# Performance work log

Hardware: AMD Instinct MI355X
Metric: run time of the kernel (lower is better)

## Reference

```python
import jax, jax.numpy as jnp
import numpy as np

EMBED = 1024
HEADS = 16
HEAD_DIM = EMBED // HEADS
SCALE = HEAD_DIM ** -0.5


def setup_inputs() -> dict:
    key = jax.random.key(0)
    ks = jax.random.split(key, 9)
    init = lambda k, shape: jax.random.normal(k, shape, dtype=jnp.float32) * 0.02
    return {
        "hidden_states": jax.random.normal(ks[0], (32, 257, EMBED), dtype=jnp.float32),
        "Wq": init(ks[1], (EMBED, EMBED)), "bq": init(ks[2], (EMBED,)),
        "Wk": init(ks[3], (EMBED, EMBED)), "bk": init(ks[4], (EMBED,)),
        "Wv": init(ks[5], (EMBED, EMBED)), "bv": init(ks[6], (EMBED,)),
        "Wo": init(ks[7], (EMBED, EMBED)), "bo": init(ks[8], (EMBED,)),
    }


def reference(hidden_states, Wq, bq, Wk, bk, Wv, bv, Wo, bo):
    b, t, d = hidden_states.shape
    # projections (torch Linear: x @ W.T + b); scale applied to Q
    q = (hidden_states @ Wq.T + bq) * SCALE
    k = hidden_states @ Wk.T + bk
    v = hidden_states @ Wv.T + bv
    # [b, h, t, hd]
    q = q.reshape(b, t, HEADS, HEAD_DIM).transpose(0, 2, 1, 3)
    k = k.reshape(b, t, HEADS, HEAD_DIM).transpose(0, 2, 1, 3)
    v = v.reshape(b, t, HEADS, HEAD_DIM).transpose(0, 2, 1, 3)
    # attention scores + softmax (dropout p is a no-op in eval mode)
    scores = jnp.einsum("bhqd,bhkd->bhqk", q, k)
    probs = jax.nn.softmax(scores, axis=-1)
    ctx = jnp.einsum("bhqk,bhkd->bhqd", probs, v)
    ctx = ctx.transpose(0, 2, 1, 3).reshape(b, t, d)
    return ctx @ Wo.T + bo
```

## Files before the change

kernel.cpp:

```cpp
#include <hip/hip_runtime.h>


#define B_   32
#define T_   257
#define TP   272
#define H_   16
#define HD_  64
#define D_   1024
#define NTOK 8224
#define BH_  512
#define FRAG_PER_BH 17408

typedef __bf16 bf16;
typedef __bf16 bf16x4 __attribute__((ext_vector_type(4)));
typedef __bf16 bf16x8 __attribute__((ext_vector_type(8)));
typedef short  s16x4  __attribute__((ext_vector_type(4)));
typedef short  s16x8  __attribute__((ext_vector_type(8)));
typedef float  floatx4 __attribute__((ext_vector_type(4)));

static constexpr size_t SZ_XB   = (size_t)NTOK * D_ * 2;
static constexpr size_t SZ_WQKV = (size_t)3 * D_ * D_ * 2;
static constexpr size_t SZ_W    = (size_t)D_ * D_ * 2;
static constexpr size_t SZ_QK   = (size_t)BH_ * FRAG_PER_BH * 2;

static constexpr size_t OFF_XB   = 0;
static constexpr size_t OFF_WQKV = OFF_XB + SZ_XB;
static constexpr size_t OFF_WO   = OFF_WQKV + SZ_WQKV;
static constexpr size_t OFF_Q    = OFF_WO + SZ_W;
static constexpr size_t OFF_K    = OFF_Q + SZ_QK;
static constexpr size_t OFF_V    = OFF_K + SZ_QK;
static constexpr size_t OFF_CTX  = OFF_V + SZ_QK;

#define GLD16(gp, lp)                                                        \
  __builtin_amdgcn_global_load_lds(                                          \
      (const __attribute__((address_space(1))) void*)(gp),                   \
      (__attribute__((address_space(3))) void*)(lp), 16, 0, 0)

__global__ void cast_all_kernel(const float* __restrict__ hs,
                                const float* __restrict__ Wq, const float* __restrict__ Wk,
                                const float* __restrict__ Wv, const float* __restrict__ Wo,
                                bf16* __restrict__ xb, bf16* __restrict__ wqkv,
                                bf16* __restrict__ wob) {
  const int y = blockIdx.y;
  const float* s;
  bf16* d;
  int n4;
  if (y == 0) {
    s = hs; d = xb; n4 = NTOK * D_ / 4;
  } else {
    int z = y - 1;
    s = (z == 0) ? Wq : (z == 1) ? Wk : (z == 2) ? Wv : Wo;
    d = (z < 3) ? wqkv + (size_t)z * D_ * D_ : wob;
    n4 = D_ * D_ / 4;
  }
  int i = blockIdx.x * blockDim.x + threadIdx.x;
  int stride = gridDim.x * blockDim.x;
  for (int idx = i; idx < n4; idx += stride) {
    float4 v = reinterpret_cast<const float4*>(s)[idx];
    bf16x4 o;
    o[0] = (bf16)v.x; o[1] = (bf16)v.y; o[2] = (bf16)v.z; o[3] = (bf16)v.w;
    reinterpret_cast<bf16x4*>(d)[idx] = o;
  }
}



#define PH_MFMA(ACC, AF, BF)                                                 \
  do {                                                                       \
    __builtin_amdgcn_s_setprio(1);                                           \
    _Pragma("unroll") for (int mi_ = 0; mi_ < 4; mi_++)                      \
      _Pragma("unroll") for (int nj_ = 0; nj_ < 2; nj_++)                    \
        _Pragma("unroll") for (int ks_ = 0; ks_ < 2; ks_++)                  \
          ACC[mi_][nj_] = __builtin_amdgcn_mfma_f32_16x16x32_bf16(           \
              AF[mi_][ks_], BF[nj_][ks_], ACC[mi_][nj_], 0, 0, 0);           \
    __builtin_amdgcn_s_setprio(0);                                           \
  } while (0)

#define READ_A(BASE)                                                         \
  do {                                                                       \
    _Pragma("unroll") for (int mi_ = 0; mi_ < 4; mi_++)                      \
      _Pragma("unroll") for (int ks_ = 0; ks_ < 2; ks_++)                    \
        af[mi_][ks_] = *reinterpret_cast<const bf16x8*>(                     \
            smem + (BASE) + aoffs[mi_][ks_]);                                \
  } while (0)

#define READ_B(DST, BASE)                                                    \
  do {                                                                       \
    _Pragma("unroll") for (int nj_ = 0; nj_ < 2; nj_++)                      \
      _Pragma("unroll") for (int ks_ = 0; ks_ < 2; ks_++)                    \
        DST[nj_][ks_] = *reinterpret_cast<const bf16x8*>(                    \
            smem + (BASE) + boffs[nj_][ks_]);                                \
  } while (0)

#define LGKM0                                                                \
  do {                                                                       \
    asm volatile("s_waitcnt lgkmcnt(0)" ::: "memory");                       \
    __builtin_amdgcn_sched_barrier(0);                                       \
  } while (0)

#define TILE4(TT, BB)                                                        \
  do {                                                                       \
    const int ktn_ = ((TT) + 2 < 16) ? (TT) + 2 : 15;                        \
                        \
    READ_A((BB) * 16384);                                                    \
    READ_B(bf0, 32768 + (BB) * 16384);                                       \
    asm volatile("s_waitcnt lgkmcnt(8)" ::: "memory");                       \
    __builtin_amdgcn_s_barrier();                                            \
    LGKM0;                                                                   \
    PH_MFMA(acc00, af, bf0);                                                 \
    __builtin_amdgcn_s_barrier();                                            \
          \
    READ_B(bf1, 32768 + (BB) * 16384 + 8192);                                \
    stageA(BB, 0, ktn_);                                                     \
    stageB(BB, 0, ktn_);                                                     \
    __builtin_amdgcn_s_barrier();                                            \
    LGKM0;                                                                   \
    PH_MFMA(acc01, af, bf1);                                                 \
    __builtin_amdgcn_s_barrier();                                            \
                                       \
    READ_A((BB) * 16384 + 8192);                                             \
    stageB(BB, 1, ktn_);                                                     \
    __builtin_amdgcn_s_barrier();                                            \
    LGKM0;                                                                   \
    PH_MFMA(acc11, af, bf1);                                                 \
    __builtin_amdgcn_s_barrier();                                            \
              \
    stageA(BB, 1, ktn_);                                                     \
    __builtin_amdgcn_sched_barrier(0);                                       \
    PH_MFMA(acc10, af, bf0);                                                 \
    asm volatile("s_waitcnt vmcnt(8)" ::: "memory");                         \
    __builtin_amdgcn_s_barrier();                                            \
  } while (0)

#define EPI_WRITE(ACC_MH0, ACC_MH1, NH)                                      \
  do {                                                                       \
    float bv_[2];                                                            \
    bv_[0] = bias[znb + (NH) * 128 + wc2 * 32 + n15];                        \
    bv_[1] = bias[znb + (NH) * 128 + wc2 * 32 + 16 + n15];                   \
    _Pragma("unroll") for (int mi_ = 0; mi_ < 4; mi_++)                      \
      _Pragma("unroll") for (int nj_ = 0; nj_ < 2; nj_++)                    \
        _Pragma("unroll") for (int r_ = 0; r_ < 4; r_++) {                   \
          int rowL_ = wr2 * 64 + mi_ * 16 + quad * 4 + r_;                   \
          int colL_ = wc2 * 32 + nj_ * 16 + n15;                             \
          smem[rowL_ * 136 + colL_] =                                        \
              (bf16)((ACC_MH0[mi_][nj_][r_] + bv_[nj_]) * scale);            \
          smem[(128 + rowL_) * 136 + colL_] =                                \
              (bf16)((ACC_MH1[mi_][nj_][r_] + bv_[nj_]) * scale);            \
        }                                                                    \
  } while (0)

__global__ __launch_bounds__(512, 2) void qkv_gemm(
    const bf16* __restrict__ xb, const bf16* __restrict__ wqkv,
    const float* __restrict__ bq, const float* __restrict__ bk,
    const float* __restrict__ bv,
    bf16* __restrict__ Qf, bf16* __restrict__ Kf, bf16* __restrict__ Vf) {
  __shared__ bf16 smem[65536];

  const int linear = blockIdx.x;
  const int mt = linear / 12, nt = linear % 12;
  const int m0 = mt * 256, n0 = nt * 256;
  const int tid = threadIdx.x;
  const int lane = tid & 63, w = tid >> 6;
  const int n15 = lane & 15, quad = lane >> 4;
  const int wr2 = w >> 2, wc2 = w & 3;
  const int srow = lane >> 3, sseg = lane & 7;

  auto stageA = [&](int buf, int half, int kt) {
#pragma unroll
    for (int c = 0; c < 2; c++) {
      int r = (w * 2 + c) * 8 + srow;
      int gm = m0 + half * 128 + r; if (gm > NTOK - 1) gm = NTOK - 1;
      int sg = (sseg ^ srow) * 8;
      GLD16(xb + (size_t)gm * D_ + kt * 64 + sg,
            smem + buf * 16384 + half * 8192 + (w * 2 + c) * 512);
    }
  };
  auto stageB = [&](int buf, int half, int kt) {
#pragma unroll
    for (int c = 0; c < 2; c++) {
      int r = (w * 2 + c) * 8 + srow;
      int gn = n0 + half * 128 + r;
      int sg = (sseg ^ srow) * 8;
      GLD16(wqkv + (size_t)gn * D_ + kt * 64 + sg,
            smem + 32768 + buf * 16384 + half * 8192 + (w * 2 + c) * 512);
    }
  };

  int aoffs[4][2], boffs[2][2];
#pragma unroll
  for (int mi = 0; mi < 4; mi++)
#pragma unroll
    for (int ks = 0; ks < 2; ks++) {
      int rh = wr2 * 64 + mi * 16 + n15;
      aoffs[mi][ks] = rh * 64 + ((ks * 4 + quad) ^ (n15 & 7)) * 8;
    }
#pragma unroll
  for (int nj = 0; nj < 2; nj++)
#pragma unroll
    for (int ks = 0; ks < 2; ks++) {
      int rh = wc2 * 32 + nj * 16 + n15;
      boffs[nj][ks] = rh * 64 + ((ks * 4 + quad) ^ (n15 & 7)) * 8;
    }

  floatx4 acc00[4][2] = {}, acc01[4][2] = {}, acc10[4][2] = {}, acc11[4][2] = {};
  bf16x8 af[4][2], bf0[2][2], bf1[2][2];

  stageA(0, 0, 0); stageB(0, 0, 0); stageB(0, 1, 0); stageA(0, 1, 0);
  stageA(1, 0, 1); stageB(1, 0, 1); stageB(1, 1, 1); stageA(1, 1, 1);
  asm volatile("s_waitcnt vmcnt(8)" ::: "memory");
  __builtin_amdgcn_s_barrier();

  for (int t = 0; t < 16; t += 2) {
    TILE4(t, 0);
    TILE4(t + 1, 1);
  }

  asm volatile("s_waitcnt vmcnt(0)" ::: "memory");
  __builtin_amdgcn_s_barrier();

  const int z = nt >> 2;
  bf16* zdst = (z == 0) ? Qf : (z == 1) ? Kf : Vf;
  const float scale = (z == 0) ? 0.125f : 1.0f;
  const float* bias = (z == 0) ? bq : (z == 1) ? bk : bv;
  const int znb = (nt & 3) * 256;

  const int mEnd = (m0 + 256 < NTOK) ? m0 + 256 : NTOK;
  const int span = mEnd - m0;
  const int bA = m0 / T_;
  const int tA = m0 - bA * T_;
  const int tEndA = (tA + span < T_) ? tA + span : T_;
  const int tgA0 = tA >> 4;
  const int nA = ((tEndA - 1) >> 4) - tgA0 + 1;
  int nU = nA, tEndB = 0;
  if (tA + span > T_ && bA + 1 < B_) {
    tEndB = tA + span - T_;
    nU += ((tEndB - 1) >> 4) + 1;
  }

  auto epi_store = [&](int nh_) {
    const int h0 = (nt & 3) * 4 + nh_ * 2;
    for (int u = w; u < nU * 2; u += 8) {
      int g = u >> 1, hh = u & 1;
      int bb, tg, tlo, thi;
      if (g < nA) {
        bb = bA; tg = tgA0 + g;
        tlo = (tA > tg * 16) ? tA : tg * 16;
        int te = tg * 16 + 16; thi = (te < tEndA) ? te : tEndA;
      } else {
        bb = bA + 1; tg = g - nA; tlo = tg * 16;
        int te = tg * 16 + 16; thi = (te < tEndB) ? te : tEndB;
      }
      bf16* gb = zdst + (size_t)(bb * H_ + h0 + hh) * FRAG_PER_BH + tg * 1024;
      const int hc = hh * 64;
      if (z != 2) {
        int ki = lane & 15, dc = lane >> 4;
        int tt = tg * 16 + ki;
        if (tt >= tlo && tt < thi) {
          int rowL = bb * T_ + tt - m0;
          bf16x8 v0 = *reinterpret_cast<const bf16x8*>(smem + rowL * 136 + hc + dc * 8);
          bf16x8 v1 = *reinterpret_cast<const bf16x8*>(smem + rowL * 136 + hc + 32 + dc * 8);
          *reinterpret_cast<bf16x8*>(gb + dc * 128 + ki * 8) = v0;
          *reinterpret_cast<bf16x8*>(gb + 512 + dc * 128 + ki * 8) = v1;
        }
      } else {
        int q2 = (lane >> 4) & 3, d16 = lane & 15;
        int tb = tg * 16 + q2 * 4;
        bool full = (tb >= tlo) && (tb + 3 < thi);
#pragma unroll
        for (int p = 0; p < 2; p++) {
          bf16x8 vv;
#pragma unroll
          for (int dp = 0; dp < 2; dp++)
#pragma unroll
            for (int ki = 0; ki < 4; ki++) {
              int tt = tb + ki;
              int rr = (bb * T_ + tt - m0) & 255;
              vv[dp * 4 + ki] = smem[rr * 136 + hc + p * 32 + dp * 16 + d16];
            }
          bf16* cp = gb + (p * 4 + q2) * 128 + d16 * 8;
          if (full) {
            *reinterpret_cast<bf16x8*>(cp) = vv;
          } else {
#pragma unroll
            for (int dp = 0; dp < 2; dp++)
#pragma unroll
              for (int ki = 0; ki < 4; ki++) {
                int tt = tb + ki;
                if (tt >= tlo && tt < thi) cp[dp * 4 + ki] = vv[dp * 4 + ki];
              }
          }
        }
      }
    }
  };

  EPI_WRITE(acc00, acc10, 0);
  __syncthreads();
  epi_store(0);
  __syncthreads();
  EPI_WRITE(acc01, acc11, 1);
  __syncthreads();
  epi_store(1);
}

__global__ __launch_bounds__(256) void attn_kernel(
    const bf16* __restrict__ Qf, const bf16* __restrict__ Kf,
    const bf16* __restrict__ Vf, bf16* __restrict__ ctx) {
  __shared__ bf16 smem[34816];

  const int bh = blockIdx.x;
  const int tid = threadIdx.x;
  const int lane = tid & 63, w = tid >> 6;
  const int n15 = lane & 15, quad = lane >> 4;
  const int b = bh >> 4, h = bh & 15;

  const bf16* Qb = Qf + (size_t)bh * FRAG_PER_BH;
  const bf16* Kb = Kf + (size_t)bh * FRAG_PER_BH;
  const bf16* Vb = Vf + (size_t)bh * FRAG_PER_BH;

#pragma unroll
  for (int j = 0; j < 17; j++) {
    int c = w * 17 + j;
    const bf16* src = (c < 34) ? (Kb + c * 512) : (Vb + (c - 34) * 512);
    GLD16(src + lane * 8, smem + c * 512);
  }
  __syncthreads();
  const bf16* Ksh = smem;
  const bf16* Vsh = smem + 17408;

  const int fo = quad * 128 + n15 * 8;

  for (int qt = w; qt < 17; qt += 4) {
    bf16x8 qb0 = *reinterpret_cast<const bf16x8*>(Qb + qt * 1024 + fo);
    bf16x8 qb1 = *reinterpret_cast<const bf16x8*>(Qb + qt * 1024 + 512 + fo);

    floatx4 s[17];
#pragma unroll
    for (int kt = 0; kt < 17; kt++) {
      bf16x8 ka0 = *reinterpret_cast<const bf16x8*>(Ksh + kt * 1024 + fo);
      bf16x8 ka1 = *reinterpret_cast<const bf16x8*>(Ksh + kt * 1024 + 512 + fo);
      floatx4 c = {};
      c = __builtin_amdgcn_mfma_f32_16x16x32_bf16(ka0, qb0, c, 0, 0, 0);
      c = __builtin_amdgcn_mfma_f32_16x16x32_bf16(ka1, qb1, c, 0, 0, 0);
      s[kt] = c;
    }
    s[16][1] = -1e30f; s[16][2] = -1e30f; s[16][3] = -1e30f;
    if (quad != 0) s[16][0] = -1e30f;

    float m0 = -1e30f;
#pragma unroll
    for (int kt = 0; kt < 17; kt++)
#pragma unroll
      for (int r = 0; r < 4; r++) m0 = fmaxf(m0, s[kt][r]);
    m0 = fmaxf(m0, __shfl_xor(m0, 16));
    m0 = fmaxf(m0, __shfl_xor(m0, 32));

    float sum = 0.f;
    s16x4 pb[17];
#pragma unroll
    for (int kt = 0; kt < 17; kt++) {
      bf16x4 ph;
#pragma unroll
      for (int r = 0; r < 4; r++) {
        float p = __expf(s[kt][r] - m0);
        sum += p;
        ph[r] = (bf16)p;
      }
      pb[kt] = __builtin_bit_cast(s16x4, ph);
    }
    sum += __shfl_xor(sum, 16);
    sum += __shfl_xor(sum, 32);

    floatx4 o[4] = {};
#pragma unroll
    for (int kt = 0; kt < 17; kt++) {
#pragma unroll
      for (int p = 0; p < 2; p++) {
        bf16x8 vv = *reinterpret_cast<const bf16x8*>(
            Vsh + ((kt * 2 + p) * 4 + quad) * 128 + n15 * 8);
        s16x8 v16 = __builtin_bit_cast(s16x8, vv);
        s16x4 vlo = __builtin_shufflevector(v16, v16, 0, 1, 2, 3);
        s16x4 vhi = __builtin_shufflevector(v16, v16, 4, 5, 6, 7);
        o[p * 2]     = __builtin_amdgcn_mfma_f32_16x16x16bf16_1k(vlo, pb[kt], o[p * 2], 0, 0, 0);
        o[p * 2 + 1] = __builtin_amdgcn_mfma_f32_16x16x16bf16_1k(vhi, pb[kt], o[p * 2 + 1], 0, 0, 0);
      }
    }

    int q = qt * 16 + n15;
    if (q < T_) {
      float inv = 1.0f / sum;
      size_t ob = ((size_t)(b * T_ + q)) * D_ + h * 64 + quad * 4;
#pragma unroll
      for (int dt = 0; dt < 4; dt++) {
        bf16x4 ov;
#pragma unroll
        for (int r = 0; r < 4; r++) ov[r] = (bf16)(o[dt][r] * inv);
        *reinterpret_cast<bf16x4*>(ctx + ob + dt * 16) = ov;
      }
    }
  }
}

__global__ __launch_bounds__(256) void o_gemm(
    const bf16* __restrict__ ctx, const bf16* __restrict__ wo,
    const float* __restrict__ bo, float* __restrict__ out) {
  __shared__ bf16 Ash[128 * 32];
  __shared__ bf16 Bsh[128 * 32];

  const int linear = blockIdx.x;
  const int nbase = (linear & 7) * 128;
  const int mbase = (linear >> 3) * 128;
  const int tid = threadIdx.x;
  const int lane = tid & 63;
  const int w = tid >> 6;
  const int wr = w >> 1, wc = w & 1;
  const int n15 = lane & 15, quad = lane >> 4;

  const int lrow = lane >> 2;
  const int lseg = (lane & 3) * 8;

  floatx4 acc[4][4] = {};

  for (int k0 = 0; k0 < D_; k0 += 32) {
#pragma unroll
    for (int c = 0; c < 2; c++) {
      int r0 = w * 32 + c * 16;
      int row = r0 + lrow;
      int gm = mbase + row; if (gm > NTOK - 1) gm = NTOK - 1;
      GLD16(ctx + (size_t)gm * D_ + k0 + lseg, Ash + r0 * 32);
      GLD16(wo + (size_t)(nbase + row) * D_ + k0 + lseg, Bsh + r0 * 32);
    }
    __syncthreads();
    bf16x8 af[4], bfr[4];
#pragma unroll
    for (int i = 0; i < 4; i++) {
      af[i]  = *reinterpret_cast<const bf16x8*>(Ash + (wr * 64 + i * 16 + n15) * 32 + quad * 8);
      bfr[i] = *reinterpret_cast<const bf16x8*>(Bsh + (wc * 64 + i * 16 + n15) * 32 + quad * 8);
    }
#pragma unroll
    for (int i = 0; i < 4; i++)
#pragma unroll
      for (int j = 0; j < 4; j++)
        acc[i][j] = __builtin_amdgcn_mfma_f32_16x16x32_bf16(af[i], bfr[j], acc[i][j], 0, 0, 0);
    __syncthreads();
  }

#pragma unroll
  for (int i = 0; i < 4; i++) {
    int rowb = mbase + wr * 64 + i * 16 + quad * 4;
#pragma unroll
    for (int j = 0; j < 4; j++) {
      int col = nbase + wc * 64 + j * 16 + n15;
      float bval = bo[col];
#pragma unroll
      for (int r = 0; r < 4; r++) {
        int m = rowb + r;
        if (m < NTOK) out[(size_t)m * D_ + col] = acc[i][j][r] + bval;
      }
    }
  }
}

extern "C" void kernel_launch(void* const* d_in, const int* in_sizes, int n_in,
                              void* d_out, int out_size, void* d_ws, size_t ws_size,
                              hipStream_t stream) {
  const float* hs = (const float*)d_in[0];
  const float* Wq = (const float*)d_in[1];
  const float* bq = (const float*)d_in[2];
  const float* Wk = (const float*)d_in[3];
  const float* bk = (const float*)d_in[4];
  const float* Wv = (const float*)d_in[5];
  const float* bv = (const float*)d_in[6];
  const float* Wo = (const float*)d_in[7];
  const float* bo = (const float*)d_in[8];

  char* ws = (char*)d_ws;
  bf16* xb   = (bf16*)(ws + OFF_XB);
  bf16* wqkv = (bf16*)(ws + OFF_WQKV);
  bf16* wob  = (bf16*)(ws + OFF_WO);
  bf16* Qfw  = (bf16*)(ws + OFF_Q);
  bf16* Kfw  = (bf16*)(ws + OFF_K);
  bf16* Vfw  = (bf16*)(ws + OFF_V);
  bf16* ctx  = (bf16*)(ws + OFF_CTX);

  cast_all_kernel<<<dim3(512, 5), 256, 0, stream>>>(hs, Wq, Wk, Wv, Wo,
                                                    xb, wqkv, wob);

  qkv_gemm<<<396, 512, 0, stream>>>(xb, wqkv, bq, bk, bv, Qfw, Kfw, Vfw);
  attn_kernel<<<BH_, 256, 0, stream>>>(Qfw, Kfw, Vfw, ctx);
  o_gemm<<<520, 256, 0, stream>>>(ctx, wob, bo, (float*)d_out);
}
```

Baseline: 236.1 us.

## Retile QKV GEMM to 256x128 tiles with smaller K-step and higher occupancy

Rewrites the QKV projection GEMM to use 256x128 output tiles with a 32-wide K step, a simpler double-buffered load/compute loop and 48KB shared memory, so four blocks can be resident per CU instead of two. The grid doubles to 792 blocks for better CU balance. The epilogue is split into two 128-row halves that reuse the smaller shared buffer. The trade-off is less data reuse per tile, more barriers per K, and the loss of the previous fine-grained interleaved phase schedule.

```diff
diff --git a/kernel.cpp b/kernel.cpp
--- a/kernel.cpp
+++ b/kernel.cpp
@@ -65,180 +65,121 @@
 
 
 
-#define PH_MFMA(ACC, AF, BF)                                                 \
+#define KTILE(TT, CC)                                                        \
   do {                                                                       \
+    const int ktn_ = ((TT) + 2 < 32) ? (TT) + 2 : 31;                        \
+    _Pragma("unroll") for (int mi_ = 0; mi_ < 4; mi_++)                      \
+      af[mi_] = *reinterpret_cast<const bf16x8*>(                            \
+          smem + (CC) * 8192 + (arow + mi_ * 16) * 32 + quad * 8);           \
+    _Pragma("unroll") for (int nj_ = 0; nj_ < 4; nj_++)                      \
+      bfr[nj_] = *reinterpret_cast<const bf16x8*>(                           \
+          smem + 16384 + (CC) * 4096 + (brow + nj_ * 16) * 32 + quad * 8);   \
+    asm volatile("s_waitcnt lgkmcnt(0)" ::: "memory");                       \
+    __builtin_amdgcn_sched_barrier(0);                                       \
+    __builtin_amdgcn_s_barrier();                                            \
+                       \
+    GLD16(aSrc0 + ktn_ * 32, dstA0 + (CC) * 8192);                           \
+    GLD16(aSrc1 + ktn_ * 32, dstA1 + (CC) * 8192);                           \
+    GLD16(bSrc + ktn_ * 32, dstB + (CC) * 4096);                             \
+    __builtin_amdgcn_sched_barrier(0);                                       \
     __builtin_amdgcn_s_setprio(1);                                           \
     _Pragma("unroll") for (int mi_ = 0; mi_ < 4; mi_++)                      \
-      _Pragma("unroll") for (int nj_ = 0; nj_ < 2; nj_++)                    \
-        _Pragma("unroll") for (int ks_ = 0; ks_ < 2; ks_++)                  \
-          ACC[mi_][nj_] = __builtin_amdgcn_mfma_f32_16x16x32_bf16(           \
-              AF[mi_][ks_], BF[nj_][ks_], ACC[mi_][nj_], 0, 0, 0);           \
+      _Pragma("unroll") for (int nj_ = 0; nj_ < 4; nj_++)                    \
+        acc[mi_][nj_] = __builtin_amdgcn_mfma_f32_16x16x32_bf16(             \
+            af[mi_], bfr[nj_], acc[mi_][nj_], 0, 0, 0);                      \
     __builtin_amdgcn_s_setprio(0);                                           \
-  } while (0)
-
-#define READ_A(BASE)                                                         \
-  do {                                                                       \
-    _Pragma("unroll") for (int mi_ = 0; mi_ < 4; mi_++)                      \
-      _Pragma("unroll") for (int ks_ = 0; ks_ < 2; ks_++)                    \
-        af[mi_][ks_] = *reinterpret_cast<const bf16x8*>(                     \
-            smem + (BASE) + aoffs[mi_][ks_]);                                \
-  } while (0)
-
-#define READ_B(DST, BASE)                                                    \
-  do {                                                                       \
-    _Pragma("unroll") for (int nj_ = 0; nj_ < 2; nj_++)                      \
-      _Pragma("unroll") for (int ks_ = 0; ks_ < 2; ks_++)                    \
-        DST[nj_][ks_] = *reinterpret_cast<const bf16x8*>(                    \
-            smem + (BASE) + boffs[nj_][ks_]);                                \
-  } while (0)
-
-#define LGKM0                                                                \
-  do {                                                                       \
-    asm volatile("s_waitcnt lgkmcnt(0)" ::: "memory");                       \
-    __builtin_amdgcn_sched_barrier(0);                                       \
-  } while (0)
-
-#define TILE4(TT, BB)                                                        \
-  do {                                                                       \
-    const int ktn_ = ((TT) + 2 < 16) ? (TT) + 2 : 15;                        \
-                        \
-    READ_A((BB) * 16384);                                                    \
-    READ_B(bf0, 32768 + (BB) * 16384);                                       \
-    asm volatile("s_waitcnt lgkmcnt(8)" ::: "memory");                       \
-    __builtin_amdgcn_s_barrier();                                            \
-    LGKM0;                                                                   \
-    PH_MFMA(acc00, af, bf0);                                                 \
-    __builtin_amdgcn_s_barrier();                                            \
-          \
-    READ_B(bf1, 32768 + (BB) * 16384 + 8192);                                \
-    stageA(BB, 0, ktn_);                                                     \
-    stageB(BB, 0, ktn_);                                                     \
-    __builtin_amdgcn_s_barrier();                                            \
-    LGKM0;                                                                   \
-    PH_MFMA(acc01, af, bf1);                                                 \
-    __builtin_amdgcn_s_barrier();                                            \
-                                       \
-    READ_A((BB) * 16384 + 8192);                                             \
-    stageB(BB, 1, ktn_);                                                     \
-    __builtin_amdgcn_s_barrier();                                            \
-    LGKM0;                                                                   \
-    PH_MFMA(acc11, af, bf1);                                                 \
-    __builtin_amdgcn_s_barrier();                                            \
-              \
-    stageA(BB, 1, ktn_);                                                     \
-    __builtin_amdgcn_sched_barrier(0);                                       \
-    PH_MFMA(acc10, af, bf0);                                                 \
-    asm volatile("s_waitcnt vmcnt(8)" ::: "memory");                         \
+    asm volatile("s_waitcnt vmcnt(3)" ::: "memory");                         \
     __builtin_amdgcn_s_barrier();                                            \
   } while (0)
 
-#define EPI_WRITE(ACC_MH0, ACC_MH1, NH)                                      \
-  do {                                                                       \
-    float bv_[2];                                                            \
-    bv_[0] = bias[znb + (NH) * 128 + wc2 * 32 + n15];                        \
-    bv_[1] = bias[znb + (NH) * 128 + wc2 * 32 + 16 + n15];                   \
-    _Pragma("unroll") for (int mi_ = 0; mi_ < 4; mi_++)                      \
-      _Pragma("unroll") for (int nj_ = 0; nj_ < 2; nj_++)                    \
-        _Pragma("unroll") for (int r_ = 0; r_ < 4; r_++) {                   \
-          int rowL_ = wr2 * 64 + mi_ * 16 + quad * 4 + r_;                   \
-          int colL_ = wc2 * 32 + nj_ * 16 + n15;                             \
-          smem[rowL_ * 136 + colL_] =                                        \
-              (bf16)((ACC_MH0[mi_][nj_][r_] + bv_[nj_]) * scale);            \
-          smem[(128 + rowL_) * 136 + colL_] =                                \
-              (bf16)((ACC_MH1[mi_][nj_][r_] + bv_[nj_]) * scale);            \
-        }                                                                    \
-  } while (0)
-
-__global__ __launch_bounds__(512, 2) void qkv_gemm(
+__global__ __launch_bounds__(512, 4) void qkv_gemm(
     const bf16* __restrict__ xb, const bf16* __restrict__ wqkv,
     const float* __restrict__ bq, const float* __restrict__ bk,
     const float* __restrict__ bv,
     bf16* __restrict__ Qf, bf16* __restrict__ Kf, bf16* __restrict__ Vf) {
-  __shared__ bf16 smem[65536];
+  __shared__ bf16 smem[24576];
 
   const int linear = blockIdx.x;
-  const int mt = linear / 12, nt = linear % 12;
-  const int m0 = mt * 256, n0 = nt * 256;
+  const int mt = linear / 24, nt = linear % 24;
+  const int m0 = mt * 256, n0 = nt * 128;
   const int tid = threadIdx.x;
   const int lane = tid & 63, w = tid >> 6;
   const int n15 = lane & 15, quad = lane >> 4;
-  const int wr2 = w >> 2, wc2 = w & 3;
-  const int srow = lane >> 3, sseg = lane & 7;
-
-  auto stageA = [&](int buf, int half, int kt) {
-#pragma unroll
-    for (int c = 0; c < 2; c++) {
-      int r = (w * 2 + c) * 8 + srow;
-      int gm = m0 + half * 128 + r; if (gm > NTOK - 1) gm = NTOK - 1;
-      int sg = (sseg ^ srow) * 8;
-      GLD16(xb + (size_t)gm * D_ + kt * 64 + sg,
-            smem + buf * 16384 + half * 8192 + (w * 2 + c) * 512);
-    }
-  };
-  auto stageB = [&](int buf, int half, int kt) {
-#pragma unroll
-    for (int c = 0; c < 2; c++) {
-      int r = (w * 2 + c) * 8 + srow;
-      int gn = n0 + half * 128 + r;
-      int sg = (sseg ^ srow) * 8;
-      GLD16(wqkv + (size_t)gn * D_ + kt * 64 + sg,
-            smem + 32768 + buf * 16384 + half * 8192 + (w * 2 + c) * 512);
-    }
-  };
-
-  int aoffs[4][2], boffs[2][2];
-#pragma unroll
-  for (int mi = 0; mi < 4; mi++)
-#pragma unroll
-    for (int ks = 0; ks < 2; ks++) {
-      int rh = wr2 * 64 + mi * 16 + n15;
-      aoffs[mi][ks] = rh * 64 + ((ks * 4 + quad) ^ (n15 & 7)) * 8;
-    }
-#pragma unroll
-  for (int nj = 0; nj < 2; nj++)
-#pragma unroll
-    for (int ks = 0; ks < 2; ks++) {
-      int rh = wc2 * 32 + nj * 16 + n15;
-      boffs[nj][ks] = rh * 64 + ((ks * 4 + quad) ^ (n15 & 7)) * 8;
-    }
-
-  floatx4 acc00[4][2] = {}, acc01[4][2] = {}, acc10[4][2] = {}, acc11[4][2] = {};
-  bf16x8 af[4][2], bf0[2][2], bf1[2][2];
-
-  stageA(0, 0, 0); stageB(0, 0, 0); stageB(0, 1, 0); stageA(0, 1, 0);
-  stageA(1, 0, 1); stageB(1, 0, 1); stageB(1, 1, 1); stageA(1, 1, 1);
-  asm volatile("s_waitcnt vmcnt(8)" ::: "memory");
+  const int wr4 = w >> 1, wn = w & 1;
+
+  const int arow = wr4 * 64 + n15;
+  const int brow = wn * 64 + n15;
+
+  const int srow = lane >> 2, sseg = (lane & 3) * 8;
+  int gmA0 = m0 + (w * 2 + 0) * 16 + srow; if (gmA0 > NTOK - 1) gmA0 = NTOK - 1;
+  int gmA1 = m0 + (w * 2 + 1) * 16 + srow; if (gmA1 > NTOK - 1) gmA1 = NTOK - 1;
+  const bf16* aSrc0 = xb + (size_t)gmA0 * D_ + sseg;
+  const bf16* aSrc1 = xb + (size_t)gmA1 * D_ + sseg;
+  const bf16* bSrc  = wqkv + (size_t)(n0 + w * 16 + srow) * D_ + sseg;
+  bf16* dstA0 = smem + (w * 2 + 0) * 512;
+  bf16* dstA1 = smem + (w * 2 + 1) * 512;
+  bf16* dstB  = smem + 16384 + w * 512;
+
+  floatx4 acc[4][4] = {};
+  bf16x8 af[4], bfr[4];
+
+  GLD16(aSrc0, dstA0); GLD16(aSrc1, dstA1); GLD16(bSrc, dstB);
+  GLD16(aSrc0 + 32, dstA0 + 8192); GLD16(aSrc1 + 32, dstA1 + 8192);
+  GLD16(bSrc + 32, dstB + 4096);
+  asm volatile("s_waitcnt vmcnt(3)" ::: "memory");
   __builtin_amdgcn_s_barrier();
 
-  for (int t = 0; t < 16; t += 2) {
-    TILE4(t, 0);
-    TILE4(t + 1, 1);
+  for (int t = 0; t < 32; t += 2) {
+    KTILE(t, 0);
+    KTILE(t + 1, 1);
   }
 
   asm volatile("s_waitcnt vmcnt(0)" ::: "memory");
   __builtin_amdgcn_s_barrier();
 
-  const int z = nt >> 2;
+  const int z = nt >> 3;
   bf16* zdst = (z == 0) ? Qf : (z == 1) ? Kf : Vf;
   const float scale = (z == 0) ? 0.125f : 1.0f;
   const float* bias = (z == 0) ? bq : (z == 1) ? bk : bv;
-  const int znb = (nt & 3) * 256;
-
-  const int mEnd = (m0 + 256 < NTOK) ? m0 + 256 : NTOK;
-  const int span = mEnd - m0;
-  const int bA = m0 / T_;
-  const int tA = m0 - bA * T_;
-  const int tEndA = (tA + span < T_) ? tA + span : T_;
-  const int tgA0 = tA >> 4;
-  const int nA = ((tEndA - 1) >> 4) - tgA0 + 1;
-  int nU = nA, tEndB = 0;
-  if (tA + span > T_ && bA + 1 < B_) {
-    tEndB = tA + span - T_;
-    nU += ((tEndB - 1) >> 4) + 1;
-  }
-
-  auto epi_store = [&](int nh_) {
-    const int h0 = (nt & 3) * 4 + nh_ * 2;
+  const int znb = (nt & 7) * 128;
+
+  for (int h = 0; h < 2; h++) {
+    if ((wr4 >> 1) == h) {
+      float bvv[4];
+#pragma unroll
+      for (int nj = 0; nj < 4; nj++)
+        bvv[nj] = bias[znb + wn * 64 + nj * 16 + n15];
+#pragma unroll
+      for (int mi = 0; mi < 4; mi++)
+#pragma unroll
+        for (int nj = 0; nj < 4; nj++) {
+          int colL = wn * 64 + nj * 16 + n15;
+#pragma unroll
+          for (int r = 0; r < 4; r++) {
+            int rowL = (wr4 & 1) * 64 + mi * 16 + quad * 4 + r;
+            smem[rowL * 136 + colL] = (bf16)((acc[mi][nj][r] + bvv[nj]) * scale);
+          }
+        }
+    }
+    __syncthreads();
+
+    const int mh0 = m0 + h * 128;
+    int nU = 0, nA = 0, tgA0 = 0, tA = 0, tEndA = 0, tEndB = 0, bA = 0;
+    int span = NTOK - mh0;
+    if (span > 0) {
+      if (span > 128) span = 128;
+      bA = mh0 / T_;
+      tA = mh0 - bA * T_;
+      tEndA = (tA + span < T_) ? tA + span : T_;
+      tgA0 = tA >> 4;
+      nA = ((tEndA - 1) >> 4) - tgA0 + 1;
+      nU = nA;
+      if (tA + span > T_ && bA + 1 < B_) {
+        tEndB = tA + span - T_;
+        nU += ((tEndB - 1) >> 4) + 1;
+      }
+    }
+
     for (int u = w; u < nU * 2; u += 8) {
       int g = u >> 1, hh = u & 1;
       int bb, tg, tlo, thi;
@@ -250,13 +191,14 @@
         bb = bA + 1; tg = g - nA; tlo = tg * 16;
         int te = tg * 16 + 16; thi = (te < tEndB) ? te : tEndB;
       }
-      bf16* gb = zdst + (size_t)(bb * H_ + h0 + hh) * FRAG_PER_BH + tg * 1024;
+      const int hgl = (nt & 7) * 2 + hh;
+      bf16* gb = zdst + (size_t)(bb * H_ + hgl) * FRAG_PER_BH + tg * 1024;
       const int hc = hh * 64;
       if (z != 2) {
         int ki = lane & 15, dc = lane >> 4;
         int tt = tg * 16 + ki;
         if (tt >= tlo && tt < thi) {
-          int rowL = bb * T_ + tt - m0;
+          int rowL = bb * T_ + tt - mh0;
           bf16x8 v0 = *reinterpret_cast<const bf16x8*>(smem + rowL * 136 + hc + dc * 8);
           bf16x8 v1 = *reinterpret_cast<const bf16x8*>(smem + rowL * 136 + hc + 32 + dc * 8);
           *reinterpret_cast<bf16x8*>(gb + dc * 128 + ki * 8) = v0;
@@ -274,7 +216,7 @@
 #pragma unroll
             for (int ki = 0; ki < 4; ki++) {
               int tt = tb + ki;
-              int rr = (bb * T_ + tt - m0) & 255;
+              int rr = (bb * T_ + tt - mh0) & 127;
               vv[dp * 4 + ki] = smem[rr * 136 + hc + p * 32 + dp * 16 + d16];
             }
           bf16* cp = gb + (p * 4 + q2) * 128 + d16 * 8;
@@ -292,15 +234,8 @@
         }
       }
     }
-  };
-
-  EPI_WRITE(acc00, acc10, 0);
-  __syncthreads();
-  epi_store(0);
-  __syncthreads();
-  EPI_WRITE(acc01, acc11, 1);
-  __syncthreads();
-  epi_store(1);
+    __syncthreads();
+  }
 }
 
 __global__ __launch_bounds__(256) void attn_kernel(
@@ -486,7 +421,7 @@
   cast_all_kernel<<<dim3(512, 5), 256, 0, stream>>>(hs, Wq, Wk, Wv, Wo,
                                                     xb, wqkv, wob);
 
-  qkv_gemm<<<396, 512, 0, stream>>>(xb, wqkv, bq, bk, bv, Qfw, Kfw, Vfw);
+  qkv_gemm<<<792, 512, 0, stream>>>(xb, wqkv, bq, bk, bv, Qfw, Kfw, Vfw);
   attn_kernel<<<BH_, 256, 0, stream>>>(Qfw, Kfw, Vfw, ctx);
   o_gemm<<<520, 256, 0, stream>>>(ctx, wob, bo, (float*)d_out);
 }
```

Result: no change. 240.1 us (+1.7%).
